# Kernel optimization log

Measured on AMD Instinct MI355X. Metric: run time of the kernel, lower is better.

## Reference

```python
import jax, jax.numpy as jnp
import numpy as np

EPS = 1e-5
GROUPS = 32

def group_norm(x, gamma, beta):
    B, C, H, W = x.shape
    g = x.reshape(B, GROUPS, C // GROUPS, H, W)
    mu = g.mean(axis=(2, 3, 4), keepdims=True)
    var = g.var(axis=(2, 3, 4), keepdims=True)
    g = (g - mu) * jax.lax.rsqrt(var + EPS)
    x = g.reshape(B, C, H, W)
    return x * gamma[None, :, None, None] + beta[None, :, None, None]

def setup_inputs() -> dict:
    key = jax.random.key(0)
    ks = jax.random.split(key, 6)
    C = 512
    x = jax.random.normal(ks[0], (16, C, 32, 32), dtype=jnp.float32)
    gamma = jnp.ones((C,), jnp.float32)
    beta = jnp.zeros((C,), jnp.float32)
    w_qkv = jax.random.normal(ks[1], (3 * C, C), jnp.float32) / np.sqrt(C)
    b_qkv = jnp.zeros((3 * C,), jnp.float32)
    w_proj = jax.random.normal(ks[2], (C, C), jnp.float32) / np.sqrt(C)
    b_proj = jnp.zeros((C,), jnp.float32)
    return {"x": x, "gamma": gamma, "beta": beta, "w_qkv": w_qkv,
            "b_qkv": b_qkv, "w_proj": w_proj, "b_proj": b_proj}

def reference(x, gamma, beta, w_qkv, b_qkv, w_proj, b_proj):
    B, C, H, W = x.shape
    h = group_norm(x, gamma, beta)
    # 1x1 conv == per-pixel linear over channels
    qkv = jnp.einsum('bchw,oc->bohw', h, w_qkv) + b_qkv[None, :, None, None]
    q, k, v = jnp.split(qkv, 3, axis=1)
    N = H * W
    q = q.reshape(B, C, N)            # [B,C,N]
    k = k.reshape(B, C, N)
    v = v.reshape(B, C, N)
    attn = jnp.einsum('bci,bcj->bij', q, k) / jnp.sqrt(jnp.float32(C))
    attn = jax.nn.softmax(attn, axis=-1)          # [B,N,N]
    out = jnp.einsum('bij,bcj->bci', attn, v)     # [B,C,N]
    out = out.reshape(B, C, H, W)
    out = jnp.einsum('bchw,oc->bohw', out, w_proj) + b_proj[None, :, None, None]
    return x + out
```

## Files before the change

### kernel.cpp

```cpp
#include <hip/hip_runtime.h>
#include <hip/hip_bf16.h>

#define BATCH 16
#define CH    512
#define NPIX  1024
#define GRP   32
#define CPG   16

typedef __attribute__((ext_vector_type(8))) short bf16x8;
typedef __attribute__((ext_vector_type(4))) float f32x4;

__device__ __forceinline__ ushort f2b(float f) {
    union { float f; unsigned u; } v; v.f = f;
    unsigned u = v.u;
    u += 0x7FFF + ((u >> 16) & 1);
    return (ushort)(u >> 16);
}

#define GLD16(gp, lp) __builtin_amdgcn_global_load_lds( \
    (__attribute__((address_space(1))) void*)(gp), \
    (__attribute__((address_space(3))) void*)(lp), 16, 0, 0)

__global__ __launch_bounds__(256) void convert_weights(
    const float* __restrict__ wq, const float* __restrict__ wp,
    ushort* __restrict__ wq_b, ushort* __restrict__ wp_b,
    float* __restrict__ rowsum) {
    int i = blockIdx.x * 256 + threadIdx.x;
    if (i < 786432) wq_b[i] = f2b(wq[i]);
    else            wp_b[i - 786432] = f2b(wp[i - 786432]);
    if (i < BATCH * NPIX) rowsum[i] = 0.f;
}

__global__ __launch_bounds__(256) void gn_stats(
    const float* __restrict__ x, float* __restrict__ mu, float* __restrict__ rs) {
    int g = blockIdx.x, b = blockIdx.y;
    const float4* p = (const float4*)(x + ((size_t)b * CH + g * CPG) * NPIX);
    float s = 0.f, ss = 0.f;
    for (int i = threadIdx.x; i < 4096; i += 256) {
        float4 v = p[i];
        s  += v.x + v.y + v.z + v.w;
        ss += v.x*v.x + v.y*v.y + v.z*v.z + v.w*v.w;
    }
    for (int o = 1; o < 64; o <<= 1) { s += __shfl_xor(s, o); ss += __shfl_xor(ss, o); }
    __shared__ float as[4], bs[4];
    int w = threadIdx.x >> 6;
    if ((threadIdx.x & 63) == 0) { as[w] = s; bs[w] = ss; }
    __syncthreads();
    if (threadIdx.x == 0) {
        s  = as[0] + as[1] + as[2] + as[3];
        ss = bs[0] + bs[1] + bs[2] + bs[3];
        float m = s * (1.0f / 16384.0f);
        float var = ss * (1.0f / 16384.0f) - m * m;
        mu[b * GRP + g] = m;
        rs[b * GRP + g] = rsqrtf(var + 1e-5f);
    }
}

__global__ __launch_bounds__(256) void gn_norm_t(
    const float* __restrict__ x, const float* __restrict__ mu, const float* __restrict__ rs,
    const float* __restrict__ gamma, const float* __restrict__ beta, ushort* __restrict__ hT) {
    int c0 = blockIdx.x * 32, n0 = blockIdx.y * 128, b = blockIdx.z;
    __shared__ ushort t[128 * 32];
    int tid = threadIdx.x;
#pragma unroll
    for (int i = 0; i < 4; i++) {
        int f = tid + i * 256;
        int c = f >> 5, nf = f & 31;
        int cg = c0 + c;
        float m = mu[b * GRP + (cg >> 4)], r = rs[b * GRP + (cg >> 4)];
        float ga = gamma[cg] * r;
        float be = beta[cg] - m * ga;
        float4 v = *(const float4*)(x + ((size_t)(b * CH + cg)) * NPIX + n0 + nf * 4);
        float vv[4] = {v.x, v.y, v.z, v.w};
#pragma unroll
        for (int j = 0; j < 4; j++) {
            int n = nf * 4 + j;
            int pos = (c >> 3) ^ ((n >> 2) & 3);
            t[n * 32 + pos * 8 + (c & 7)] = f2b(vv[j] * ga + be);
        }
    }
    __syncthreads();
#pragma unroll
    for (int i = 0; i < 2; i++) {
        int ch = tid + i * 256;
        int n = ch >> 2, g = ch & 3;
        int pos = g ^ ((n >> 2) & 3);
        uint4 val = *(const uint4*)&t[n * 32 + pos * 8];
        *(uint4*)(hT + ((size_t)b * NPIX + n0 + n) * CH + c0 + g * 8) = val;
    }
}

#define BK 64

template<int EPI, int BMt, int BNt>
__global__ __launch_bounds__(256, 4) void gemm_bt(
    const ushort* __restrict__ A, long sA, int lda,
    const ushort* __restrict__ Bt, long sB, int ldb,
    int K,
    void* __restrict__ Out, long sO, int ldo,
    const float* __restrict__ bias,
    const float* __restrict__ resid,
    ushort* __restrict__ vout,
    float* __restrict__ rowsum,
    float scale) {
    constexpr int FM = BMt / 32;
    constexpr int FN = BNt / 32;
    constexpr int SA = BMt / 32;
    constexpr int SB = BNt / 32;
    __shared__ __align__(16) ushort sh[(BMt + BNt) * BK];
    ushort* As = sh;
    ushort* Bs = sh + BMt * BK;

    int nx = gridDim.x, ny = gridDim.y;
    int L = blockIdx.x + nx * (blockIdx.y + ny * blockIdx.z);
    int per = (nx * ny * (int)gridDim.z) >> 3;
    int wid = (L & 7) * per + (L >> 3);
    int bx = wid % nx; wid /= nx;
    int by = wid % ny;
    int b  = wid / ny;

    A  += (size_t)b * sA;
    Bt += (size_t)b * sB;
    int m0 = by * BMt, n0 = bx * BNt;
    int tid = threadIdx.x;
    int lane = tid & 63;
    int wave = tid >> 6;
    int q = lane >> 4, l = lane & 15;
    int wm = (wave >> 1) * (BMt / 2), wn = (wave & 1) * (BNt / 2);

    int aoff[SA], boff[SB], lofa[SA], lofb[SB];
#pragma unroll
    for (int i = 0; i < SA; i++) {
        int p = tid + i * 256, r = p >> 3, g = (p & 7) ^ (r & 7);
        aoff[i] = (m0 + r) * lda + g * 8;
        lofa[i] = p * 8;
    }
#pragma unroll
    for (int i = 0; i < SB; i++) {
        int p = tid + i * 256, r = p >> 3, g = (p & 7) ^ (r & 7);
        boff[i] = (n0 + r) * ldb + g * 8;
        lofb[i] = p * 8;
    }

    int offA[FM][2], offB[FN][2];
#pragma unroll
    for (int mi = 0; mi < FM; mi++) {
        int r = wm + mi * 16 + l;
#pragma unroll
        for (int kk = 0; kk < 2; kk++)
            offA[mi][kk] = r * 64 + ((((kk << 2) | q) ^ (r & 7)) * 8);
    }
#pragma unroll
    for (int ni = 0; ni < FN; ni++) {
        int r = wn + ni * 16 + l;
#pragma unroll
        for (int kk = 0; kk < 2; kk++)
            offB[ni][kk] = r * 64 + ((((kk << 2) | q) ^ (r & 7)) * 8);
    }

    f32x4 zero = {0.f, 0.f, 0.f, 0.f};
    f32x4 acc[FM][FN];
#pragma unroll
    for (int mi = 0; mi < FM; mi++)
#pragma unroll
        for (int ni = 0; ni < FN; ni++) acc[mi][ni] = zero;

    for (int k0 = 0; k0 < K; k0 += BK) {
        __syncthreads();
#pragma unroll
        for (int i = 0; i < SA; i++) GLD16(A + aoff[i] + k0, As + lofa[i]);
#pragma unroll
        for (int i = 0; i < SB; i++) GLD16(Bt + boff[i] + k0, Bs + lofb[i]);
        __syncthreads();
#pragma unroll
        for (int kk = 0; kk < 2; kk++) {
            bf16x8 af[FM], bfr[FN];
#pragma unroll
            for (int mi = 0; mi < FM; mi++) af[mi]  = *(const bf16x8*)(As + offA[mi][kk]);
#pragma unroll
            for (int ni = 0; ni < FN; ni++) bfr[ni] = *(const bf16x8*)(Bs + offB[ni][kk]);
#pragma unroll
            for (int mi = 0; mi < FM; mi++)
#pragma unroll
                for (int ni = 0; ni < FN; ni++)
                    acc[mi][ni] = __builtin_amdgcn_mfma_f32_16x16x32_bf16(
                        af[mi], bfr[ni], acc[mi][ni], 0, 0, 0);
        }
    }

    if (EPI == 0) {
        if (n0 >= 1024) {
            __syncthreads();
#pragma unroll
            for (int mi = 0; mi < FM; mi++)
#pragma unroll
                for (int ni = 0; ni < FN; ni++) {
                    int nl = wn + ni * 16 + l;
                    float bi = bias[n0 + nl];
#pragma unroll
                    for (int rg = 0; rg < 4; rg++) {
                        int ml = wm + mi * 16 + q * 4 + rg;
                        int pos = (ml >> 3) ^ (nl & 15);
                        sh[nl * 128 + pos * 8 + (ml & 7)] = f2b(acc[mi][ni][rg] + bi);
                    }
                }
            __syncthreads();
#pragma unroll
            for (int i = 0; i < 8; i++) {
                int idx = tid + i * 256;
                int nl = idx >> 4, ch = idx & 15;
                int g2 = ch ^ (nl & 15);
                uint4 val = *(const uint4*)&sh[nl * 128 + g2 * 8];
                *(uint4*)(vout + (size_t)b * (512 * 1024)
                          + (size_t)(n0 - 1024 + nl) * 1024 + m0 + ch * 8) = val;
            }
            return;
        }
#pragma unroll
        for (int mi = 0; mi < FM; mi++)
#pragma unroll
            for (int ni = 0; ni < FN; ni++) {
                int n = n0 + wn + ni * 16 + l;
                float bi = bias[n];
#pragma unroll
                for (int rg = 0; rg < 4; rg++) {
                    int m = m0 + wm + mi * 16 + q * 4 + rg;
                    ((ushort*)Out)[(size_t)b * sO + (size_t)m * ldo + n] =
                        f2b(acc[mi][ni][rg] + bi);
                }
            }
        return;
    }
    if (EPI == 1) {
#pragma unroll
        for (int mi = 0; mi < FM; mi++) {
            float rsum[4] = {0.f, 0.f, 0.f, 0.f};
#pragma unroll
            for (int ni = 0; ni < FN; ni++) {
                int n = n0 + wn + ni * 16 + l;
#pragma unroll
                for (int rg = 0; rg < 4; rg++) {
                    int m = m0 + wm + mi * 16 + q * 4 + rg;
                    float u = __expf(acc[mi][ni][rg] * scale);
                    rsum[rg] += u;
                    ((ushort*)Out)[(size_t)b * sO + (size_t)m * ldo + n] = f2b(u);
                }
            }
#pragma unroll
            for (int rg = 0; rg < 4; rg++) {
                float s = rsum[rg];
                s += __shfl_xor(s, 1); s += __shfl_xor(s, 2);
                s += __shfl_xor(s, 4); s += __shfl_xor(s, 8);
                if (l == 0)
                    atomicAdd(&rowsum[b * NPIX + m0 + wm + mi * 16 + q * 4 + rg], s);
            }
        }
        return;
    }
#pragma unroll
    for (int mi = 0; mi < FM; mi++) {
        float inv[4];
        if (EPI == 2) {
#pragma unroll
            for (int rg = 0; rg < 4; rg++)
                inv[rg] = 1.0f / rowsum[b * NPIX + m0 + wm + mi * 16 + q * 4 + rg];
        }
#pragma unroll
        for (int ni = 0; ni < FN; ni++) {
            int mbase = m0 + wm + mi * 16 + q * 4;
            int n = n0 + wn + ni * 16 + l;
#pragma unroll
            for (int rg = 0; rg < 4; rg++) {
                int m = mbase + rg;
                float v = acc[mi][ni][rg];
                if (EPI == 2) {
                    ((ushort*)Out)[(size_t)b * sO + (size_t)m * ldo + n] = f2b(v * inv[rg]);
                } else {
                    v += bias[m] + resid[(size_t)b * sO + (size_t)m * ldo + n];
                    ((float*)Out)[(size_t)b * sO + (size_t)m * ldo + n] = v;
                }
            }
        }
    }
}

extern "C" void kernel_launch(void* const* d_in, const int* in_sizes, int n_in,
                              void* d_out, int out_size, void* d_ws, size_t ws_size,
                              hipStream_t stream) {
    const float* x     = (const float*)d_in[0];
    const float* gamma = (const float*)d_in[1];
    const float* beta  = (const float*)d_in[2];
    const float* wqkv  = (const float*)d_in[3];
    const float* bqkv  = (const float*)d_in[4];
    const float* wproj = (const float*)d_in[5];
    const float* bproj = (const float*)d_in[6];
    float* out = (float*)d_out;
    char* ws = (char*)d_ws;

    ushort* wq_b   = (ushort*)(ws + 0);
    ushort* wp_b   = (ushort*)(ws + 1572864);
    float*  mu     = (float*)(ws + 2097152);
    float*  rs     = (float*)(ws + 2099200);
    float*  rowsum = (float*)(ws + 2101248);
    ushort* hT     = (ushort*)(ws + 2166784);
    ushort* qk     = (ushort*)(ws + 18944000);
    ushort* vb     = (ushort*)(ws + 52498432);
    ushort* u      = (ushort*)(ws + 69275648);
    ushort* O1T    = hT;

    convert_weights<<<4096, 256, 0, stream>>>(wqkv, wproj, wq_b, wp_b, rowsum);
    gn_stats<<<dim3(GRP, BATCH), 256, 0, stream>>>(x, mu, rs);
    gn_norm_t<<<dim3(16, 8, BATCH), 256, 0, stream>>>(x, mu, rs, gamma, beta, hT);

    gemm_bt<0, 128, 128><<<dim3(12, 8, BATCH), 256, 0, stream>>>(
        hT, 524288, 512, wq_b, 0, 512, 512,
        qk, 1048576, 1024, bqkv, nullptr, vb, nullptr, 0.f);

    gemm_bt<1, 128, 128><<<dim3(8, 8, BATCH), 256, 0, stream>>>(
        qk, 1048576, 1024, qk + 512, 1048576, 1024, 512,
        u, 1048576, 1024, nullptr, nullptr, nullptr, rowsum, 0.044194173824159216f);

    gemm_bt<2, 128, 64><<<dim3(8, 8, BATCH), 256, 0, stream>>>(
        u, 1048576, 1024, vb, 524288, 1024, 1024,
        O1T, 524288, 512, nullptr, nullptr, nullptr, rowsum, 0.f);

    gemm_bt<3, 64, 128><<<dim3(8, 8, BATCH), 256, 0, stream>>>(
        wp_b, 0, 512, O1T, 524288, 512, 512,
        out, 524288, 1024, bproj, x, nullptr, nullptr, 0.f);
}
```

Before: 212.0 us.

## Fuse QK^T, softmax and PV into a single flash-style attention kernel

Replaces the two separate GEMMs (scores with exp and atomic row sums, then P·V with normalization) with one kernel. Each block keeps 32 query rows in LDS, walks key tiles of 64, computes exp scores into a small LDS tile and accumulates P·V in registers, then normalizes by the row sums reduced in LDS. This removes the 32MB bf16 score matrix round-trip, the rowsum atomics and zero-init, and one launch. The costs are K and V read directly from global memory without LDS staging and only 512 blocks. Like the old code, it skips the max subtraction and relies on scores staying small.

```diff
diff --git a/kernel.cpp b/kernel.cpp
--- a/kernel.cpp
+++ b/kernel.cpp
@@ -23,12 +23,10 @@
 
 __global__ __launch_bounds__(256) void convert_weights(
     const float* __restrict__ wq, const float* __restrict__ wp,
-    ushort* __restrict__ wq_b, ushort* __restrict__ wp_b,
-    float* __restrict__ rowsum) {
+    ushort* __restrict__ wq_b, ushort* __restrict__ wp_b) {
     int i = blockIdx.x * 256 + threadIdx.x;
     if (i < 786432) wq_b[i] = f2b(wq[i]);
     else            wp_b[i - 786432] = f2b(wp[i - 786432]);
-    if (i < BATCH * NPIX) rowsum[i] = 0.f;
 }
 
 __global__ __launch_bounds__(256) void gn_stats(
@@ -231,40 +229,8 @@
             }
         return;
     }
-    if (EPI == 1) {
-#pragma unroll
-        for (int mi = 0; mi < FM; mi++) {
-            float rsum[4] = {0.f, 0.f, 0.f, 0.f};
-#pragma unroll
-            for (int ni = 0; ni < FN; ni++) {
-                int n = n0 + wn + ni * 16 + l;
-#pragma unroll
-                for (int rg = 0; rg < 4; rg++) {
-                    int m = m0 + wm + mi * 16 + q * 4 + rg;
-                    float u = __expf(acc[mi][ni][rg] * scale);
-                    rsum[rg] += u;
-                    ((ushort*)Out)[(size_t)b * sO + (size_t)m * ldo + n] = f2b(u);
-                }
-            }
-#pragma unroll
-            for (int rg = 0; rg < 4; rg++) {
-                float s = rsum[rg];
-                s += __shfl_xor(s, 1); s += __shfl_xor(s, 2);
-                s += __shfl_xor(s, 4); s += __shfl_xor(s, 8);
-                if (l == 0)
-                    atomicAdd(&rowsum[b * NPIX + m0 + wm + mi * 16 + q * 4 + rg], s);
-            }
-        }
-        return;
-    }
 #pragma unroll
     for (int mi = 0; mi < FM; mi++) {
-        float inv[4];
-        if (EPI == 2) {
-#pragma unroll
-            for (int rg = 0; rg < 4; rg++)
-                inv[rg] = 1.0f / rowsum[b * NPIX + m0 + wm + mi * 16 + q * 4 + rg];
-        }
 #pragma unroll
         for (int ni = 0; ni < FN; ni++) {
             int mbase = m0 + wm + mi * 16 + q * 4;
@@ -273,15 +239,126 @@
             for (int rg = 0; rg < 4; rg++) {
                 int m = mbase + rg;
                 float v = acc[mi][ni][rg];
-                if (EPI == 2) {
-                    ((ushort*)Out)[(size_t)b * sO + (size_t)m * ldo + n] = f2b(v * inv[rg]);
-                } else {
-                    v += bias[m] + resid[(size_t)b * sO + (size_t)m * ldo + n];
-                    ((float*)Out)[(size_t)b * sO + (size_t)m * ldo + n] = v;
-                }
-            }
-        }
-    }
+                v += bias[m] + resid[(size_t)b * sO + (size_t)m * ldo + n];
+                ((float*)Out)[(size_t)b * sO + (size_t)m * ldo + n] = v;
+            }
+        }
+    }
+}
+
+__global__ __launch_bounds__(256, 3) void attn_fused(
+    const ushort* __restrict__ qk, const ushort* __restrict__ vb,
+    ushort* __restrict__ o1t) {
+    __shared__ __align__(16) ushort qs[32 * 512];
+    __shared__ __align__(16) ushort ps[32 * 72];
+
+    int L = blockIdx.x + 32 * blockIdx.z;
+    int wid = (L & 7) * 64 + (L >> 3);
+    int i0 = (wid & 31) * 32;
+    int b = wid >> 5;
+
+    const ushort* qb = qk + (size_t)b * 1048576;
+    const ushort* kb = qb + 512;
+    const ushort* v  = vb + (size_t)b * (512 * 1024);
+
+    int tid = threadIdx.x, lane = tid & 63, w = tid >> 6;
+    int q = lane >> 4, l = lane & 15;
+
+#pragma unroll
+    for (int i = 0; i < 8; i++) {
+        int p = tid + i * 256, r = p >> 6, g = (p & 63) ^ (r & 7);
+        GLD16(qb + (size_t)(i0 + r) * 1024 + g * 8, qs + p * 8);
+    }
+    __syncthreads();
+
+    f32x4 zero = {0.f, 0.f, 0.f, 0.f};
+    f32x4 oacc[2][8];
+#pragma unroll
+    for (int mi = 0; mi < 2; mi++)
+#pragma unroll
+        for (int ni = 0; ni < 8; ni++) oacc[mi][ni] = zero;
+    float rsum[2][4];
+#pragma unroll
+    for (int mi = 0; mi < 2; mi++)
+#pragma unroll
+        for (int rg = 0; rg < 4; rg++) rsum[mi][rg] = 0.f;
+
+    for (int jt = 0; jt < 16; jt++) {
+        int j0 = jt * 64;
+        f32x4 sacc[2] = {zero, zero};
+        const ushort* krow = kb + (size_t)(j0 + w * 16 + l) * 1024;
+#pragma unroll
+        for (int kc = 0; kc < 16; kc++) {
+            bf16x8 kf = *(const bf16x8*)(krow + kc * 32 + q * 8);
+#pragma unroll
+            for (int mi = 0; mi < 2; mi++) {
+                int r = mi * 16 + l;
+                bf16x8 af = *(const bf16x8*)(qs + r * 512 + (((kc * 4 + q) ^ (r & 7)) * 8));
+                sacc[mi] = __builtin_amdgcn_mfma_f32_16x16x32_bf16(af, kf, sacc[mi], 0, 0, 0);
+            }
+        }
+        __syncthreads();
+#pragma unroll
+        for (int mi = 0; mi < 2; mi++)
+#pragma unroll
+            for (int rg = 0; rg < 4; rg++) {
+                float u = __expf(sacc[mi][rg] * 0.044194173824159216f);
+                rsum[mi][rg] += u;
+                ps[(mi * 16 + q * 4 + rg) * 72 + w * 16 + l] = f2b(u);
+            }
+        __syncthreads();
+        bf16x8 pf[2][2];
+#pragma unroll
+        for (int mi = 0; mi < 2; mi++)
+#pragma unroll
+            for (int kk = 0; kk < 2; kk++)
+                pf[mi][kk] = *(const bf16x8*)(ps + (mi * 16 + l) * 72 + (kk * 4 + q) * 8);
+#pragma unroll
+        for (int ni = 0; ni < 8; ni++) {
+            const ushort* vrow = v + (size_t)(w * 128 + ni * 16 + l) * 1024 + j0;
+#pragma unroll
+            for (int kk = 0; kk < 2; kk++) {
+                bf16x8 vf = *(const bf16x8*)(vrow + kk * 32 + q * 8);
+#pragma unroll
+                for (int mi = 0; mi < 2; mi++)
+                    oacc[mi][ni] = __builtin_amdgcn_mfma_f32_16x16x32_bf16(
+                        pf[mi][kk], vf, oacc[mi][ni], 0, 0, 0);
+            }
+        }
+    }
+
+    __syncthreads();
+    float* rl = (float*)ps;
+#pragma unroll
+    for (int mi = 0; mi < 2; mi++)
+#pragma unroll
+        for (int rg = 0; rg < 4; rg++) {
+            float s = rsum[mi][rg];
+            s += __shfl_xor(s, 1); s += __shfl_xor(s, 2);
+            s += __shfl_xor(s, 4); s += __shfl_xor(s, 8);
+            if (l == 0) rl[w * 32 + mi * 16 + q * 4 + rg] = s;
+        }
+    __syncthreads();
+    float inv[2][4];
+#pragma unroll
+    for (int mi = 0; mi < 2; mi++)
+#pragma unroll
+        for (int rg = 0; rg < 4; rg++) {
+            int row = mi * 16 + q * 4 + rg;
+            inv[mi][rg] = 1.0f / (rl[row] + rl[32 + row] + rl[64 + row] + rl[96 + row]);
+        }
+#pragma unroll
+    for (int mi = 0; mi < 2; mi++)
+#pragma unroll
+        for (int ni = 0; ni < 8; ni++) {
+            int c = w * 128 + ni * 16 + l;
+#pragma unroll
+            for (int rg = 0; rg < 4; rg++) {
+                int i = i0 + mi * 16 + q * 4 + rg;
+                o1t[(size_t)b * 524288 + (size_t)i * 512 + c] =
+                    f2b(oacc[mi][ni][rg] * inv[mi][rg]);
+            }
+        }
 }
 
 extern "C" void kernel_launch(void* const* d_in, const int* in_sizes, int n_in,
@@ -301,14 +378,12 @@
     ushort* wp_b   = (ushort*)(ws + 1572864);
     float*  mu     = (float*)(ws + 2097152);
     float*  rs     = (float*)(ws + 2099200);
-    float*  rowsum = (float*)(ws + 2101248);
     ushort* hT     = (ushort*)(ws + 2166784);
     ushort* qk     = (ushort*)(ws + 18944000);
     ushort* vb     = (ushort*)(ws + 52498432);
-    ushort* u      = (ushort*)(ws + 69275648);
     ushort* O1T    = hT;
 
-    convert_weights<<<4096, 256, 0, stream>>>(wqkv, wproj, wq_b, wp_b, rowsum);
+    convert_weights<<<4096, 256, 0, stream>>>(wqkv, wproj, wq_b, wp_b);
     gn_stats<<<dim3(GRP, BATCH), 256, 0, stream>>>(x, mu, rs);
     gn_norm_t<<<dim3(16, 8, BATCH), 256, 0, stream>>>(x, mu, rs, gamma, beta, hT);
 
@@ -316,13 +391,7 @@
         hT, 524288, 512, wq_b, 0, 512, 512,
         qk, 1048576, 1024, bqkv, nullptr, vb, nullptr, 0.f);
 
-    gemm_bt<1, 128, 128><<<dim3(8, 8, BATCH), 256, 0, stream>>>(
-        qk, 1048576, 1024, qk + 512, 1048576, 1024, 512,
-        u, 1048576, 1024, nullptr, nullptr, nullptr, rowsum, 0.044194173824159216f);
-
-    gemm_bt<2, 128, 64><<<dim3(8, 8, BATCH), 256, 0, stream>>>(
-        u, 1048576, 1024, vb, 524288, 1024, 1024,
-        O1T, 524288, 512, nullptr, nullptr, nullptr, rowsum, 0.f);
+    attn_fused<<<dim3(32, 1, BATCH), 256, 0, stream>>>(qk, vb, O1T);
 
     gemm_bt<3, 64, 128><<<dim3(8, 8, BATCH), 256, 0, stream>>>(
         wp_b, 0, 512, O1T, 524288, 512, 512,
```

Result: slower. 313.8 us (+48.0%).

## Fuse group-norm stats and normalize-transpose into one kernel via LDS staging

Applied to the files above, without the earlier changes.

Merges the two group-norm kernels into one. Each block loads its group's 16x1024 slice into shared memory (64 KB), reduces the mean and variance, then normalizes from LDS and writes the transposed bf16 output. This avoids a second global read of x and one kernel launch. In exchange it uses 64 KB of LDS per block, which limits occupancy, launches only 512 blocks instead of 2048, and each thread's output writes are two 16-byte stores per row at a 1 KB stride.

```diff
diff --git a/kernel.cpp b/kernel.cpp
--- a/kernel.cpp
+++ b/kernel.cpp
@@ -31,62 +31,49 @@
     if (i < BATCH * NPIX) rowsum[i] = 0.f;
 }
 
-__global__ __launch_bounds__(256) void gn_stats(
-    const float* __restrict__ x, float* __restrict__ mu, float* __restrict__ rs) {
+__global__ __launch_bounds__(256) void gn_fused(
+    const float* __restrict__ x, const float* __restrict__ gamma,
+    const float* __restrict__ beta, ushort* __restrict__ hT) {
+    __shared__ float xs[CPG * NPIX];
+    __shared__ float as[4], bs[4];
     int g = blockIdx.x, b = blockIdx.y;
     const float4* p = (const float4*)(x + ((size_t)b * CH + g * CPG) * NPIX);
+    float4* xs4 = (float4*)xs;
     float s = 0.f, ss = 0.f;
     for (int i = threadIdx.x; i < 4096; i += 256) {
         float4 v = p[i];
+        xs4[i] = v;
         s  += v.x + v.y + v.z + v.w;
         ss += v.x*v.x + v.y*v.y + v.z*v.z + v.w*v.w;
     }
     for (int o = 1; o < 64; o <<= 1) { s += __shfl_xor(s, o); ss += __shfl_xor(ss, o); }
-    __shared__ float as[4], bs[4];
     int w = threadIdx.x >> 6;
     if ((threadIdx.x & 63) == 0) { as[w] = s; bs[w] = ss; }
     __syncthreads();
-    if (threadIdx.x == 0) {
-        s  = as[0] + as[1] + as[2] + as[3];
-        ss = bs[0] + bs[1] + bs[2] + bs[3];
-        float m = s * (1.0f / 16384.0f);
-        float var = ss * (1.0f / 16384.0f) - m * m;
-        mu[b * GRP + g] = m;
-        rs[b * GRP + g] = rsqrtf(var + 1e-5f);
-    }
-}
-
-__global__ __launch_bounds__(256) void gn_norm_t(
-    const float* __restrict__ x, const float* __restrict__ mu, const float* __restrict__ rs,
-    const float* __restrict__ gamma, const float* __restrict__ beta, ushort* __restrict__ hT) {
-    int c0 = blockIdx.x * 32, n0 = blockIdx.y * 128, b = blockIdx.z;
-    __shared__ ushort t[128 * 32];
-    int tid = threadIdx.x;
+    s  = as[0] + as[1] + as[2] + as[3];
+    ss = bs[0] + bs[1] + bs[2] + bs[3];
+    float m   = s * (1.0f / 16384.0f);
+    float var = ss * (1.0f / 16384.0f) - m * m;
+    float r   = rsqrtf(var + 1e-5f);
+
+    int c0 = g * CPG;
+    float ga[CPG], be[CPG];
+#pragma unroll
+    for (int c = 0; c < CPG; c++) {
+        float gg = gamma[c0 + c] * r;
+        ga[c] = gg;
+        be[c] = beta[c0 + c] - m * gg;
+    }
+    ushort tmp[CPG];
 #pragma unroll
     for (int i = 0; i < 4; i++) {
-        int f = tid + i * 256;
-        int c = f >> 5, nf = f & 31;
-        int cg = c0 + c;
-        float m = mu[b * GRP + (cg >> 4)], r = rs[b * GRP + (cg >> 4)];
-        float ga = gamma[cg] * r;
-        float be = beta[cg] - m * ga;
-        float4 v = *(const float4*)(x + ((size_t)(b * CH + cg)) * NPIX + n0 + nf * 4);
-        float vv[4] = {v.x, v.y, v.z, v.w};
-#pragma unroll
-        for (int j = 0; j < 4; j++) {
-            int n = nf * 4 + j;
-            int pos = (c >> 3) ^ ((n >> 2) & 3);
-            t[n * 32 + pos * 8 + (c & 7)] = f2b(vv[j] * ga + be);
-        }
-    }
-    __syncthreads();
-#pragma unroll
-    for (int i = 0; i < 2; i++) {
-        int ch = tid + i * 256;
-        int n = ch >> 2, g = ch & 3;
-        int pos = g ^ ((n >> 2) & 3);
-        uint4 val = *(const uint4*)&t[n * 32 + pos * 8];
-        *(uint4*)(hT + ((size_t)b * NPIX + n0 + n) * CH + c0 + g * 8) = val;
+        int n = threadIdx.x + i * 256;
+#pragma unroll
+        for (int c = 0; c < CPG; c++)
+            tmp[c] = f2b(xs[c * NPIX + n] * ga[c] + be[c]);
+        uint4* dst = (uint4*)(hT + ((size_t)b * NPIX + n) * CH + c0);
+        dst[0] = *(const uint4*)&tmp[0];
+        dst[1] = *(const uint4*)&tmp[8];
     }
 }
 
@@ -299,8 +286,6 @@
 
     ushort* wq_b   = (ushort*)(ws + 0);
     ushort* wp_b   = (ushort*)(ws + 1572864);
-    float*  mu     = (float*)(ws + 2097152);
-    float*  rs     = (float*)(ws + 2099200);
     float*  rowsum = (float*)(ws + 2101248);
     ushort* hT     = (ushort*)(ws + 2166784);
     ushort* qk     = (ushort*)(ws + 18944000);
@@ -309,8 +294,7 @@
     ushort* O1T    = hT;
 
     convert_weights<<<4096, 256, 0, stream>>>(wqkv, wproj, wq_b, wp_b, rowsum);
-    gn_stats<<<dim3(GRP, BATCH), 256, 0, stream>>>(x, mu, rs);
-    gn_norm_t<<<dim3(16, 8, BATCH), 256, 0, stream>>>(x, mu, rs, gamma, beta, hT);
+    gn_fused<<<dim3(GRP, BATCH), 256, 0, stream>>>(x, gamma, beta, hT);
 
     gemm_bt<0, 128, 128><<<dim3(12, 8, BATCH), 256, 0, stream>>>(
         hT, 524288, 512, wq_b, 0, 512, 512,
```

Result: no change. 211.8 us, median of 2 (-0.1%).
